# Kernel optimization log

Hardware: AMD Instinct MI355X
Metric: run time of the kernel (lower is better)

## Reference

```python
import math
import jax, jax.numpy as jnp
import numpy as np

NUM_HEADS = 12
EPS = 1e-4


def softmax_kernel_features(data, proj, is_query):
    # data: [B,H,N,d], proj: [m,d] -> features [B,H,N,m]
    d = data.shape[-1]
    data_normalizer = 1.0 / math.sqrt(math.sqrt(d))
    ratio = 1.0 / math.sqrt(proj.shape[0])
    data_dash = jnp.einsum('bhnd,md->bhnm', data_normalizer * data, proj)
    diag_data = (jnp.sum(jnp.square(data), axis=-1, keepdims=True)
                 * 0.5 * data_normalizer * data_normalizer)  # [B,H,N,1]
    if is_query:
        stab = jnp.max(data_dash, axis=-1, keepdims=True)
    else:
        stab = jnp.max(data_dash)
    return ratio * (jnp.exp(data_dash - diag_data - stab) + EPS)


def setup_inputs() -> dict:
    key = jax.random.key(0)
    k0, k1, k2, k3, k4 = jax.random.split(key, 5)
    B, N, C, H = 8, 4096, 768, NUM_HEADS
    hd = C // H
    m = int(hd * math.log(hd))  # 266
    x = jax.random.normal(k0, (B, N, C), dtype=jnp.float32)
    W_qkv = jax.random.normal(k1, (C, 3 * C), dtype=jnp.float32) / math.sqrt(C)
    W_proj = jax.random.normal(k2, (C, C), dtype=jnp.float32) / math.sqrt(C)
    b_proj = jnp.zeros((C,), dtype=jnp.float32)
    proj_mat = jax.random.normal(k3, (m, hd), dtype=jnp.float32)
    return {'x': x, 'W_qkv': W_qkv, 'W_proj': W_proj, 'b_proj': b_proj,
            'proj_mat': proj_mat}


def reference(x, W_qkv, W_proj, b_proj, proj_mat):
    B, N, C = x.shape
    H = NUM_HEADS
    hd = C // H
    qkv = (x @ W_qkv).reshape(B, N, 3, H, hd)
    qkv = jnp.transpose(qkv, (2, 0, 3, 1, 4))  # [3,B,H,N,hd]
    q, k, v = qkv[0], qkv[1], qkv[2]
    q1 = softmax_kernel_features(q, proj_mat, is_query=True)   # [B,H,N,m]
    k1 = softmax_kernel_features(k, proj_mat, is_query=False)  # [B,H,N,m]
    # FAVOR+ non-causal linear attention
    kv = jnp.einsum('bhnm,bhnd->bhmd', k1, v)        # [B,H,m,hd]
    ksum = jnp.sum(k1, axis=2)                        # [B,H,m]
    z = 1.0 / jnp.einsum('bhnm,bhm->bhn', q1, ksum)  # [B,H,N]
    out = jnp.einsum('bhnm,bhmd->bhnd', q1, kv) * z[..., None]
    out = jnp.transpose(out, (0, 2, 1, 3)).reshape(B, N, C)
    return out @ W_proj + b_proj
```

## Files before the change

kernel.cpp:

```cpp
#include <hip/hip_runtime.h>
#include <hip/hip_bf16.h>
#include <math.h>

#define B_ 8
#define N_TOK 4096
#define C_ 768
#define H_ 12
#define HD_ 64
#define M_ 266
#define TC_ 2304
#define BH_ 96
#define ROWS_ 32768

#define M2 288
#define MP 296
#define KVS 72
#define K1S 40

#define DN 0.35355339059327373f
#define RATIO 0.06131393394849658f
#define FEPS 1e-4f
#define NEG_INF -3.0e38f

typedef __attribute__((ext_vector_type(4))) float f32x4;
typedef __attribute__((ext_vector_type(8))) short bf16x8;

__device__ __forceinline__ float bf2f(unsigned short u) {
  return __uint_as_float(((unsigned int)u) << 16);
}
__device__ __forceinline__ unsigned short f2bf(float f) {
  unsigned int x = __float_as_uint(f);
  unsigned int r = (x + 0x7fffu + ((x >> 16) & 1u)) >> 16;
  return (unsigned short)r;
}

#define GLOAD_LDS16(g, l) \
  __builtin_amdgcn_global_load_lds( \
      (const __attribute__((address_space(1))) void*)(g), \
      (__attribute__((address_space(3))) void*)(l), 16, 0, 0)

__global__ __launch_bounds__(256) void cast_bf16(
    const float* __restrict__ src, unsigned short* __restrict__ dst, int n)
{
  int i = (blockIdx.x * 256 + threadIdx.x) * 4;
  if (i < n) {
    float4 v = *(const float4*)&src[i];
    ushort4 u;
    u.x = f2bf(v.x); u.y = f2bf(v.y); u.z = f2bf(v.z); u.w = f2bf(v.w);
    *(ushort4*)&dst[i] = u;
  }
}

__global__ __launch_bounds__(256) void cast_pbf(
    const float* __restrict__ P, unsigned short* __restrict__ Pbf)
{
  int idx = blockIdx.x * 256 + threadIdx.x;
  if (idx < M2 * 64) {
    int m = idx >> 6;
    Pbf[idx] = (m < M_) ? f2bf(P[idx]) : (unsigned short)0;
  }
}

__global__ __launch_bounds__(256) void transpose_cast(
    const float* __restrict__ src, unsigned short* __restrict__ dst,
    int R, int Ccols)
{
  __shared__ float t[32][33];
  const int c0 = blockIdx.x * 32, r0 = blockIdx.y * 32;
  const int tx = threadIdx.x & 31, ty = threadIdx.x >> 5;
#pragma unroll
  for (int i = 0; i < 32; i += 8)
    t[ty + i][tx] = src[(size_t)(r0 + ty + i) * Ccols + c0 + tx];
  __syncthreads();
#pragma unroll
  for (int i = 0; i < 32; i += 8)
    dst[(size_t)(c0 + ty + i) * R + r0 + tx] = f2bf(t[tx][ty + i]);
}

template <int NT, int C_BF16, int HAS_BIAS>
__global__ __launch_bounds__(512) void gemm_pipe(
    const unsigned short* __restrict__ A, const unsigned short* __restrict__ Bt,
    const float* __restrict__ bias, void* __restrict__ Cptr)
{
  __shared__ unsigned short lds_[73728];
  const int Kdim = 768, Ndim = NT * 128;
  const int tid = threadIdx.x;
  const int lane = tid & 63, w = tid >> 6;

  const int id = blockIdx.x;
  const int sid = (id & 7) * (16 * NT) + (id >> 3);
  const int row0 = (sid / NT) * 256;
  const int col0 = (sid % NT) * 128;

  const int srow = w * 8 + (lane >> 3);
  const int skb = (((lane & 7) ^ ((lane >> 3) & 7)) << 4);
  const size_t agb0 = (size_t)(row0 + srow) * Kdim + (skb >> 1);
  const size_t agb1 = (size_t)(row0 + 64 + srow) * Kdim + (skb >> 1);
  const size_t agb2 = (size_t)(row0 + 128 + srow) * Kdim + (skb >> 1);
  const size_t agb3 = (size_t)(row0 + 192 + srow) * Kdim + (skb >> 1);
  const size_t bgb0 = (size_t)(col0 + srow) * Kdim + (skb >> 1);
  const size_t bgb1 = (size_t)(col0 + 64 + srow) * Kdim + (skb >> 1);
  const int al0 = 0 * 4096 + w * 512 + lane * 8;
  const int al1 = 1 * 4096 + w * 512 + lane * 8;
  const int al2 = 2 * 4096 + w * 512 + lane * 8;
  const int al3 = 3 * 4096 + w * 512 + lane * 8;
  const int bl0 = 16384 + 0 * 4096 + w * 512 + lane * 8;
  const int bl1 = 16384 + 1 * 4096 + w * 512 + lane * 8;

#define STAGE_Q(tt) do { \
    unsigned short* Lq_ = lds_ + ((tt) % 3) * 24576; \
    const int kq_ = (tt) * 64; \
    GLOAD_LDS16(A + agb0 + kq_, Lq_ + al0); \
    GLOAD_LDS16(A + agb1 + kq_, Lq_ + al1); \
    GLOAD_LDS16(A + agb2 + kq_, Lq_ + al2); \
    GLOAD_LDS16(A + agb3 + kq_, Lq_ + al3); \
    GLOAD_LDS16(Bt + bgb0 + kq_, Lq_ + bl0); \
    GLOAD_LDS16(Bt + bgb1 + kq_, Lq_ + bl1); \
  } while (0)

  const int fr = lane & 15, q = lane >> 4;
  const int wm = w >> 2, wn = w & 3;
  const int f7 = fr & 7;
  const int sl0 = ((q + 0) ^ f7) << 3;
  const int sl1 = ((q + 4) ^ f7) << 3;
  const int abase = (wm * 128 + fr) * 64;
  const int bbase0 = 16384 + (wn * 32 + fr) * 64;
  const int bbase1 = 16384 + (wn * 32 + 16 + fr) * 64;

  f32x4 acc[8][2];
  const f32x4 fz = {0.f, 0.f, 0.f, 0.f};
#pragma unroll
  for (int m = 0; m < 8; ++m) { acc[m][0] = fz; acc[m][1] = fz; }

  STAGE_Q(0);
  STAGE_Q(1);

#pragma unroll 1
  for (int t = 0; t < 12; ++t) {
    if (t < 10) STAGE_Q(t + 2);
    if (t < 10)       asm volatile("s_waitcnt vmcnt(12)" ::: "memory");
    else if (t == 10) asm volatile("s_waitcnt vmcnt(6)" ::: "memory");
    else              asm volatile("s_waitcnt vmcnt(0)" ::: "memory");
    __builtin_amdgcn_sched_barrier(0);
    __builtin_amdgcn_s_barrier();
    __builtin_amdgcn_sched_barrier(0);

    const unsigned short* Lb = lds_ + (t % 3) * 24576;
#pragma unroll
    for (int ks = 0; ks < 2; ++ks) {
      const int sl = ks ? sl1 : sl0;
      bf16x8 bv0 = *(const bf16x8*)&Lb[bbase0 + sl];
      bf16x8 bv1 = *(const bf16x8*)&Lb[bbase1 + sl];
      bf16x8 av[8];
#pragma unroll
      for (int m = 0; m < 8; ++m)
        av[m] = *(const bf16x8*)&Lb[abase + m * 1024 + sl];
      __builtin_amdgcn_s_setprio(1);
#pragma unroll
      for (int m = 0; m < 8; ++m) {
        acc[m][0] = __builtin_amdgcn_mfma_f32_16x16x32_bf16(av[m], bv0, acc[m][0], 0, 0, 0);
        acc[m][1] = __builtin_amdgcn_mfma_f32_16x16x32_bf16(av[m], bv1, acc[m][1], 0, 0, 0);
      }
      __builtin_amdgcn_s_setprio(0);
    }
    __builtin_amdgcn_sched_barrier(0);
    __builtin_amdgcn_s_barrier();
    __builtin_amdgcn_sched_barrier(0);
  }
#undef STAGE_Q

  const int orow = q * 4;
#pragma unroll
  for (int m = 0; m < 8; ++m) {
#pragma unroll
    for (int n = 0; n < 2; ++n) {
      const int c = col0 + wn * 32 + n * 16 + fr;
      float badd = 0.f;
      if constexpr (HAS_BIAS) badd = bias[c];
#pragma unroll
      for (int j = 0; j < 4; ++j) {
        const int r = row0 + wm * 128 + m * 16 + orow + j;
        float v = acc[m][n][j] + badd;
        if constexpr (C_BF16)
          ((unsigned short*)Cptr)[(size_t)r * Ndim + c] = f2bf(v);
        else
          ((float*)Cptr)[(size_t)r * Ndim + c] = v;
      }
    }
  }
}

__global__ __launch_bounds__(256) void kmax_mfma(
    const unsigned short* __restrict__ qkv, const unsigned short* __restrict__ Pbf,
    float* __restrict__ bmax)
{
  __shared__ unsigned short K_lds[2][64 * KVS];
  __shared__ float red[4];
  const int tid = threadIdx.x;
  const int w = tid >> 6, lane = tid & 63;
  const int lr = lane & 15, q = lane >> 4;
  const int bh = blockIdx.x, chunk = blockIdx.y, z = blockIdx.z;
  const int b = bh / H_, h = bh % H_;
  const int ms = z * 8 + 2 * w;
  const int mc = (z == 1 && w == 3) ? 3 : 2;
  const int sn = 16 * w + (lane >> 2);
  const int sd0 = (lane & 3) * 16;
  const f32x4 fz = {0.f, 0.f, 0.f, 0.f};
  float mx = NEG_INF;

  bf16x8 pf0[3], pf1[3];
#pragma unroll
  for (int i = 0; i < 3; ++i) {
    const unsigned short* prow = Pbf + (size_t)((ms + i) * 16 + lr) * 64 + q * 8;
    pf0[i] = *(const bf16x8*)prow;
    pf1[i] = *(const bf16x8*)(prow + 32);
  }

  const unsigned short* kbase = qkv + (size_t)(b * N_TOK + chunk * 512 + sn) * TC_ + C_ + h * HD_ + sd0;
  const size_t gstep = (size_t)64 * TC_;

  int4 ka = *(const int4*)kbase;
  int4 kb = *(const int4*)(kbase + 8);
  *(int4*)&K_lds[0][sn * KVS + sd0] = ka;
  *(int4*)&K_lds[0][sn * KVS + sd0 + 8] = kb;
  asm volatile("s_waitcnt lgkmcnt(0)" ::: "memory");
  __builtin_amdgcn_s_barrier();

#pragma unroll 1
  for (int g = 0; g < 8; ++g) {
    const unsigned short* Kc = K_lds[g & 1];
    if (g < 7) {
      const unsigned short* kr = kbase + (size_t)(g + 1) * gstep;
      ka = *(const int4*)kr;
      kb = *(const int4*)(kr + 8);
    }
    __builtin_amdgcn_sched_barrier(0);
    bf16x8 bk[4][2];
#pragma unroll
    for (int nt = 0; nt < 4; ++nt) {
      bk[nt][0] = *(const bf16x8*)&Kc[(nt * 16 + lr) * KVS + q * 8];
      bk[nt][1] = *(const bf16x8*)&Kc[(nt * 16 + lr) * KVS + 32 + q * 8];
    }
#pragma unroll
    for (int i = 0; i < 3; ++i) {
      if (i >= mc) continue;
      const int m = (ms + i) * 16 + lr;
#pragma unroll
      for (int nt = 0; nt < 4; ++nt) {
        f32x4 s = fz;
        s = __builtin_amdgcn_mfma_f32_16x16x32_bf16(bk[nt][0], pf0[i], s, 0, 0, 0);
        s = __builtin_amdgcn_mfma_f32_16x16x32_bf16(bk[nt][1], pf1[i], s, 0, 0, 0);
        if (m < M_)
          mx = fmaxf(mx, fmaxf(fmaxf(s[0], s[1]), fmaxf(s[2], s[3])));
      }
    }
    if (g < 7) {
      __builtin_amdgcn_sched_barrier(0);
      __builtin_amdgcn_s_barrier();
      unsigned short* Kn = (unsigned short*)K_lds[(g & 1) ^ 1];
      *(int4*)&Kn[sn * KVS + sd0] = ka;
      *(int4*)&Kn[sn * KVS + sd0 + 8] = kb;
      asm volatile("s_waitcnt lgkmcnt(0)" ::: "memory");
      __builtin_amdgcn_sched_barrier(0);
      __builtin_amdgcn_s_barrier();
      __builtin_amdgcn_sched_barrier(0);
    }
  }
#pragma unroll
  for (int off = 32; off >= 1; off >>= 1) mx = fmaxf(mx, __shfl_xor(mx, off));
  if (lane == 0) red[w] = mx;
  __syncthreads();
  if (tid == 0)
    bmax[(z * 8 + chunk) * BH_ + bh] = fmaxf(fmaxf(red[0], red[1]), fmaxf(red[2], red[3]));
}

__global__ __launch_bounds__(256) void kmax_reduce(
    const float* __restrict__ bmax, float* __restrict__ kmaxp, int n)
{
  __shared__ float red[4];
  float v = NEG_INF;
  for (int i = threadIdx.x; i < n; i += 256) v = fmaxf(v, bmax[i]);
#pragma unroll
  for (int off = 32; off >= 1; off >>= 1) v = fmaxf(v, __shfl_xor(v, off));
  if ((threadIdx.x & 63) == 0) red[threadIdx.x >> 6] = v;
  __syncthreads();
  if (threadIdx.x == 0)
    kmaxp[0] = DN * fmaxf(fmaxf(red[0], red[1]), fmaxf(red[2], red[3]));
}

__global__ __launch_bounds__(256) void kv_partial_mfma(
    const unsigned short* __restrict__ qkv, const unsigned short* __restrict__ Pbf,
    const float* __restrict__ kmaxp,
    float* __restrict__ kvpart, float* __restrict__ ksumpart)
{
  __shared__ unsigned short K_lds[64 * KVS];
  __shared__ unsigned short Vt_lds[64 * KVS];
  __shared__ unsigned short k1_lds[272 * K1S];
  __shared__ float diag_lds[64];
  const int tid = threadIdx.x;
  const int w = tid >> 6, lane = tid & 63;
  const int lr = lane & 15, q = lane >> 4;
  const int bh = blockIdx.x, chunk = blockIdx.y, z = blockIdx.z;
  const int b = bh / H_, h = bh % H_;
  const float stab = kmaxp[0];
  const int ms = z * 8 + 2 * w;
  const int mc = (z == 1 && w == 3) ? 3 : 2;
  const int sn = 16 * w + (lane >> 2);
  const int sd0 = (lane & 3) * 16;
  const int vswz = sn ^ ((lane & 3) << 4);
  const int kswz = (lr >> 3) << 4;
  const f32x4 fz = {0.f, 0.f, 0.f, 0.f};

  f32x4 kvacc[3][4];
  float ksacc[3];
#pragma unroll
  for (int i = 0; i < 3; ++i) {
    ksacc[i] = 0.f;
#pragma unroll
    for (int dt = 0; dt < 4; ++dt) kvacc[i][dt] = fz;
  }

  bf16x8 pf0[3], pf1[3];
#pragma unroll
  for (int i = 0; i < 3; ++i) {
    const unsigned short* prow = Pbf + (size_t)((ms + i) * 16 + lr) * 64 + q * 8;
    pf0[i] = *(const bf16x8*)prow;
    pf1[i] = *(const bf16x8*)(prow + 32);
  }

  const unsigned short* kbase = qkv + (size_t)(b * N_TOK + chunk * 512 + sn) * TC_ + C_ + h * HD_ + sd0;
  const size_t gstep = (size_t)64 * TC_;

  auto write_buf = [&](int4 wka, int4 wkb, int4 wva, int4 wvb) {
    *(int4*)&K_lds[sn * KVS + sd0] = wka;
    *(int4*)&K_lds[sn * KVS + sd0 + 8] = wkb;
    float sq = 0.f;
    const unsigned short* pk0 = (const unsigned short*)&wka;
#pragma unroll
    for (int j = 0; j < 8; ++j) { float f = bf2f(pk0[j]); sq = fmaf(f, f, sq); }
    const unsigned short* pk1 = (const unsigned short*)&wkb;
#pragma unroll
    for (int j = 0; j < 8; ++j) { float f = bf2f(pk1[j]); sq = fmaf(f, f, sq); }
    sq += __shfl_xor(sq, 1);
    sq += __shfl_xor(sq, 2);
    if ((lane & 3) == 0) diag_lds[sn] = 0.0625f * sq;
    const unsigned short* pv0 = (const unsigned short*)&wva;
    const unsigned short* pv1 = (const unsigned short*)&wvb;
#pragma unroll
    for (int j = 0; j < 8; ++j) Vt_lds[(sd0 + j) * KVS + vswz] = pv0[j];
#pragma unroll
    for (int j = 0; j < 8; ++j) Vt_lds[(sd0 + 8 + j) * KVS + vswz] = pv1[j];
  };

  int4 ka = *(const int4*)kbase;
  int4 kb = *(const int4*)(kbase + 8);
  int4 va = *(const int4*)(kbase + C_);
  int4 vb = *(const int4*)(kbase + C_ + 8);
  write_buf(ka, kb, va, vb);
  asm volatile("s_waitcnt lgkmcnt(0)" ::: "memory");
  __builtin_amdgcn_s_barrier();

#pragma unroll 1
  for (int g = 0; g < 8; ++g) {
    if (g < 7) {
      const unsigned short* kr = kbase + (size_t)(g + 1) * gstep;
      ka = *(const int4*)kr;
      kb = *(const int4*)(kr + 8);
      va = *(const int4*)(kr + C_);
      vb = *(const int4*)(kr + C_ + 8);
    }
    __builtin_amdgcn_sched_barrier(0);

#pragma unroll
    for (int ks = 0; ks < 2; ++ks) {
      bf16x8 bkl[2][2];
#pragma unroll
      for (int t = 0; t < 2; ++t) {
        const int nrow = ((2 * ks + t) * 16 + lr) * KVS;
        bkl[t][0] = *(const bf16x8*)&K_lds[nrow + q * 8];
        bkl[t][1] = *(const bf16x8*)&K_lds[nrow + 32 + q * 8];
      }
      bf16x8 bv[4];
#pragma unroll
      for (int dt = 0; dt < 4; ++dt)
        bv[dt] = *(const bf16x8*)&Vt_lds[(dt * 16 + lr) * KVS + ((ks * 32 + q * 8) ^ (dt << 4))];

#pragma unroll
      for (int i = 0; i < 3; ++i) {
        if (i >= mc) continue;
        const int mt = ms + i;
        const int m = mt * 16 + lr;
        const int mrow = (mt * 16 + lr) * K1S;
        float loc = 0.f;
#pragma unroll
        for (int t = 0; t < 2; ++t) {
          f32x4 s = fz;
          s = __builtin_amdgcn_mfma_f32_16x16x32_bf16(bkl[t][0], pf0[i], s, 0, 0, 0);
          s = __builtin_amdgcn_mfma_f32_16x16x32_bf16(bkl[t][1], pf1[i], s, 0, 0, 0);
          ushort4 uo;
          unsigned short* puo = (unsigned short*)&uo;
#pragma unroll
          for (int j = 0; j < 4; ++j) {
            const int nl = (2 * ks + t) * 16 + q * 4 + j;
            float k1f = 0.f;
            if (m < M_) {
              float dash = DN * s[j];
              k1f = RATIO * (__expf(dash - diag_lds[nl] - stab) + FEPS);
            }
            loc += k1f;
            puo[j] = f2bf(k1f);
          }
          *(ushort4*)&k1_lds[mrow + ((t * 16 + q * 4) ^ kswz)] = uo;
        }
        ksacc[i] += loc;
        bf16x8 a1 = *(const bf16x8*)&k1_lds[mrow + ((q * 8) ^ kswz)];
#pragma unroll
        for (int dt = 0; dt < 4; ++dt)
          kvacc[i][dt] = __builtin_amdgcn_mfma_f32_16x16x32_bf16(a1, bv[dt], kvacc[i][dt], 0, 0, 0);
      }
    }

    if (g < 7) {
      __builtin_amdgcn_sched_barrier(0);
      __builtin_amdgcn_s_barrier();
      __builtin_amdgcn_sched_barrier(0);
      write_buf(ka, kb, va, vb);
      asm volatile("s_waitcnt lgkmcnt(0)" ::: "memory");
      __builtin_amdgcn_sched_barrier(0);
      __builtin_amdgcn_s_barrier();
      __builtin_amdgcn_sched_barrier(0);
    }
  }

  const size_t cb = (size_t)(chunk * BH_ + bh) * 64;
#pragma unroll
  for (int i = 0; i < 3; ++i) {
    if (i >= mc) continue;
    const int mt = ms + i;
#pragma unroll
    for (int dt = 0; dt < 4; ++dt) {
      float4 v4;
      v4.x = kvacc[i][dt][0]; v4.y = kvacc[i][dt][1];
      v4.z = kvacc[i][dt][2]; v4.w = kvacc[i][dt][3];
      *(float4*)&kvpart[(cb + dt * 16 + lr) * M2 + mt * 16 + q * 4] = v4;
    }
    float s = ksacc[i];
    s += __shfl_xor(s, 16);
    s += __shfl_xor(s, 32);
    if (lane < 16)
      ksumpart[(size_t)(chunk * BH_ + bh) * M2 + mt * 16 + lane] = s;
  }
}

__global__ __launch_bounds__(256) void kv_reduce2(
    const float* __restrict__ kvpart, const float* __restrict__ ksumpart,
    unsigned short* __restrict__ kvt_g, float* __restrict__ ksum_g)
{
  const int KVN = BH_ * 64 * M2;
  const int KSN = BH_ * M2;
  int idx = blockIdx.x * 256 + threadIdx.x;
  if (idx < KVN) {
    int m = idx % M2;
    float s = 0.f;
    if (m < M_) {
#pragma unroll
      for (int c = 0; c < 8; ++c) s += kvpart[(size_t)c * KVN + idx];
    }
    kvt_g[idx] = f2bf(s);
  } else if (idx < KVN + KSN) {
    int j = idx - KVN;
    int m = j % M2;
    float s = 0.f;
    if (m < M_) {
#pragma unroll
      for (int c = 0; c < 8; ++c) s += ksumpart[(size_t)c * KSN + j];
    }
    ksum_g[j] = s;
  }
}

__global__ __launch_bounds__(256) void attn_mfma(
    const unsigned short* __restrict__ qkv, const unsigned short* __restrict__ Pbf,
    const unsigned short* __restrict__ kvt_g, const float* __restrict__ ksum_g,
    unsigned short* __restrict__ attn)
{
  __shared__ unsigned short q1_lds[64 * MP];
  __shared__ unsigned short kvt_lds[64 * MP];
  __shared__ float ksum_lds[M2];
  __shared__ float z_lds[64];
  const int tid = threadIdx.x;
  const int bh = blockIdx.x, qt = blockIdx.y;
  const int b = bh / H_, h = bh % H_;
  const int n0 = qt * 64;
  const int w = tid >> 6, lane = tid & 63;
  const int lr = lane & 15, q = lane >> 4;

  {
    const unsigned short* src = kvt_g + (size_t)bh * 64 * M2;
#pragma unroll
    for (int i = 0; i < 9; ++i) {
      int chunk = i * 256 + tid;
      int r = chunk / 36, c = (chunk % 36) * 8;
      *(int4*)&kvt_lds[r * MP + c] = *(const int4*)(src + r * M2 + c);
    }
    if (tid < 72)
      *(float4*)&ksum_lds[tid * 4] = *(const float4*)(ksum_g + (size_t)bh * M2 + tid * 4);
    if (tid < 64) {
      const int4 z4 = {0, 0, 0, 0};
      *(int4*)&q1_lds[tid * MP + 272] = z4;
      *(int4*)&q1_lds[tid * MP + 280] = z4;
    }
  }
  __syncthreads();

  const unsigned short* qrow = qkv + (size_t)(b * N_TOK + n0 + w * 16 + lr) * TC_ + h * HD_;
  bf16x8 bq0 = *(const bf16x8*)(qrow + q * 8);
  bf16x8 bq1 = *(const bf16x8*)(qrow + q * 8 + 32);
  float sq = 0.f;
  {
    const unsigned short* p0 = (const unsigned short*)&bq0;
    const unsigned short* p1 = (const unsigned short*)&bq1;
#pragma unroll
    for (int j = 0; j < 8; ++j) { float f = bf2f(p0[j]); sq = fmaf(f, f, sq); }
#pragma unroll
    for (int j = 0; j < 8; ++j) { float f = bf2f(p1[j]); sq = fmaf(f, f, sq); }
  }
  sq += __shfl_xor(sq, 16);
  sq += __shfl_xor(sq, 32);
  const float diag = 0.0625f * sq;

  f32x4 sacc[17];
  const f32x4 fz = {0.f, 0.f, 0.f, 0.f};
#pragma unroll
  for (int mt = 0; mt < 17; ++mt) sacc[mt] = fz;
#pragma unroll
  for (int mt = 0; mt < 17; ++mt) {
    const unsigned short* prow = Pbf + (size_t)(mt * 16 + lr) * 64;
    bf16x8 ap0 = *(const bf16x8*)(prow + q * 8);
    bf16x8 ap1 = *(const bf16x8*)(prow + q * 8 + 32);
    sacc[mt] = __builtin_amdgcn_mfma_f32_16x16x32_bf16(ap0, bq0, sacc[mt], 0, 0, 0);
    sacc[mt] = __builtin_amdgcn_mfma_f32_16x16x32_bf16(ap1, bq1, sacc[mt], 0, 0, 0);
  }

  float mxr = NEG_INF;
#pragma unroll
  for (int mt = 0; mt < 17; ++mt) {
#pragma unroll
    for (int j = 0; j < 4; ++j) {
      int m = mt * 16 + q * 4 + j;
      if (m < M_) mxr = fmaxf(mxr, sacc[mt][j]);
    }
  }
  mxr = fmaxf(mxr, __shfl_xor(mxr, 16));
  mxr = fmaxf(mxr, __shfl_xor(mxr, 32));
  const float mxd = DN * mxr;

  float zp = 0.f;
#pragma unroll
  for (int mt = 0; mt < 17; ++mt) {
    ushort4 uo;
    unsigned short* puo = (unsigned short*)&uo;
#pragma unroll
    for (int j = 0; j < 4; ++j) {
      const int m = mt * 16 + q * 4 + j;
      float q1f = 0.f;
      if (m < M_) {
        float dash = DN * sacc[mt][j];
        q1f = RATIO * (__expf(dash - diag - mxd) + FEPS);
      }
      zp = fmaf(q1f, ksum_lds[m], zp);
      puo[j] = f2bf(q1f);
    }
    *(ushort4*)&q1_lds[(w * 16 + lr) * MP + mt * 16 + q * 4] = uo;
  }
  zp += __shfl_xor(zp, 16);
  zp += __shfl_xor(zp, 32);
  if (q == 0) z_lds[w * 16 + lr] = 1.0f / zp;

  f32x4 oacc[4];
#pragma unroll
  for (int dt = 0; dt < 4; ++dt) oacc[dt] = fz;
#pragma unroll
  for (int ks = 0; ks < 9; ++ks) {
    bf16x8 aq = *(const bf16x8*)&q1_lds[(w * 16 + lr) * MP + ks * 32 + q * 8];
#pragma unroll
    for (int dt = 0; dt < 4; ++dt) {
      bf16x8 bkv = *(const bf16x8*)&kvt_lds[(dt * 16 + lr) * MP + ks * 32 + q * 8];
      oacc[dt] = __builtin_amdgcn_mfma_f32_16x16x32_bf16(aq, bkv, oacc[dt], 0, 0, 0);
    }
  }

  float zz[4];
#pragma unroll
  for (int j = 0; j < 4; ++j) zz[j] = z_lds[w * 16 + q * 4 + j];
#pragma unroll
  for (int dt = 0; dt < 4; ++dt) {
#pragma unroll
    for (int j = 0; j < 4; ++j) {
      const int r = b * N_TOK + n0 + w * 16 + q * 4 + j;
      attn[(size_t)r * C_ + h * HD_ + dt * 16 + lr] = f2bf(oacc[dt][j] * zz[j]);
    }
  }
}

extern "C" void kernel_launch(void* const* d_in, const int* in_sizes, int n_in,
                              void* d_out, int out_size, void* d_ws, size_t ws_size,
                              hipStream_t stream) {
  const float* x     = (const float*)d_in[0];
  const float* Wqkv  = (const float*)d_in[1];
  const float* Wproj = (const float*)d_in[2];
  const float* bproj = (const float*)d_in[3];
  const float* P     = (const float*)d_in[4];
  float* out = (float*)d_out;
  float* ws = (float*)d_ws;

  unsigned short* qkv    = (unsigned short*)ws;
  unsigned short* xb     = (unsigned short*)(ws + 37748736);
  float*          kvpart = ws + 37748736;
  unsigned short* attn   = (unsigned short*)(ws + 37748736);
  float* ksumpart = ws + 51904512;
  unsigned short* kvt_g  = (unsigned short*)(ws + 52125696);
  float* ksum_g   = ws + 53010432;
  float* bmax     = ws + 53038080;
  float* kmaxp    = ws + 53041152;
  unsigned short* Pbf    = (unsigned short*)(ws + 53041216);
  unsigned short* Wqkvt  = (unsigned short*)(ws + 53050432);
  unsigned short* Wprojt = (unsigned short*)(ws + 53935168);

  cast_bf16<<<dim3(24576), 256, 0, stream>>>(x, xb, ROWS_ * C_);
  transpose_cast<<<dim3(72, 24), 256, 0, stream>>>(Wqkv, Wqkvt, C_, TC_);
  transpose_cast<<<dim3(24, 24), 256, 0, stream>>>(Wproj, Wprojt, C_, C_);
  cast_pbf<<<dim3(72), 256, 0, stream>>>(P, Pbf);

  gemm_pipe<18, 1, 0><<<dim3(2304), 512, 0, stream>>>(xb, Wqkvt, nullptr, qkv);
  kmax_mfma<<<dim3(96, 8, 2), 256, 0, stream>>>(qkv, Pbf, bmax);
  kmax_reduce<<<dim3(1), 256, 0, stream>>>(bmax, kmaxp, 1536);
  kv_partial_mfma<<<dim3(96, 8, 2), 256, 0, stream>>>(qkv, Pbf, kmaxp, kvpart, ksumpart);
  kv_reduce2<<<dim3(7020), 256, 0, stream>>>(kvpart, ksumpart, kvt_g, ksum_g);
  attn_mfma<<<dim3(96, 64), 256, 0, stream>>>(qkv, Pbf, kvt_g, ksum_g, attn);
  gemm_pipe<6, 0, 1><<<dim3(768), 512, 0, stream>>>(attn, Wprojt, bproj, out);
}
```

Before: 539.3 us.

## Widen GEMM tiles to 256x256 with double-buffered LDS staging

```diff
diff --git a/kernel.cpp b/kernel.cpp
--- a/kernel.cpp
+++ b/kernel.cpp
@@ -82,40 +82,40 @@
     const unsigned short* __restrict__ A, const unsigned short* __restrict__ Bt,
     const float* __restrict__ bias, void* __restrict__ Cptr)
 {
-  __shared__ unsigned short lds_[73728];
-  const int Kdim = 768, Ndim = NT * 128;
+  __shared__ unsigned short lds_[65536];
+  const int Kdim = 768, Ndim = NT * 256;
   const int tid = threadIdx.x;
   const int lane = tid & 63, w = tid >> 6;
 
   const int id = blockIdx.x;
-  const int sid = (id & 7) * (16 * NT) + (id >> 3);
+  const int nwg8 = (128 * NT) >> 3;
+  const int sid = (id & 7) * nwg8 + (id >> 3);
   const int row0 = (sid / NT) * 256;
-  const int col0 = (sid % NT) * 128;
-
-  const int srow = w * 8 + (lane >> 3);
-  const int skb = (((lane & 7) ^ ((lane >> 3) & 7)) << 4);
-  const size_t agb0 = (size_t)(row0 + srow) * Kdim + (skb >> 1);
-  const size_t agb1 = (size_t)(row0 + 64 + srow) * Kdim + (skb >> 1);
-  const size_t agb2 = (size_t)(row0 + 128 + srow) * Kdim + (skb >> 1);
-  const size_t agb3 = (size_t)(row0 + 192 + srow) * Kdim + (skb >> 1);
-  const size_t bgb0 = (size_t)(col0 + srow) * Kdim + (skb >> 1);
-  const size_t bgb1 = (size_t)(col0 + 64 + srow) * Kdim + (skb >> 1);
-  const int al0 = 0 * 4096 + w * 512 + lane * 8;
-  const int al1 = 1 * 4096 + w * 512 + lane * 8;
-  const int al2 = 2 * 4096 + w * 512 + lane * 8;
-  const int al3 = 3 * 4096 + w * 512 + lane * 8;
-  const int bl0 = 16384 + 0 * 4096 + w * 512 + lane * 8;
-  const int bl1 = 16384 + 1 * 4096 + w * 512 + lane * 8;
+  const int col0 = (sid % NT) * 256;
+
+  const int srow = tid >> 3;
+  const int skb = (((tid & 7) ^ (srow & 7)) << 4);
+  const size_t ag0 = (size_t)(row0 + srow) * Kdim + (skb >> 1);
+  const size_t ag1 = (size_t)(row0 + 64 + srow) * Kdim + (skb >> 1);
+  const size_t ag2 = (size_t)(row0 + 128 + srow) * Kdim + (skb >> 1);
+  const size_t ag3 = (size_t)(row0 + 192 + srow) * Kdim + (skb >> 1);
+  const size_t bg0 = (size_t)(col0 + srow) * Kdim + (skb >> 1);
+  const size_t bg1 = (size_t)(col0 + 64 + srow) * Kdim + (skb >> 1);
+  const size_t bg2 = (size_t)(col0 + 128 + srow) * Kdim + (skb >> 1);
+  const size_t bg3 = (size_t)(col0 + 192 + srow) * Kdim + (skb >> 1);
+  const int dst = tid * 8;
 
 #define STAGE_Q(tt) do { \
-    unsigned short* Lq_ = lds_ + ((tt) % 3) * 24576; \
+    unsigned short* Lq_ = lds_ + ((tt) & 1) * 32768; \
     const int kq_ = (tt) * 64; \
-    GLOAD_LDS16(A + agb0 + kq_, Lq_ + al0); \
-    GLOAD_LDS16(A + agb1 + kq_, Lq_ + al1); \
-    GLOAD_LDS16(A + agb2 + kq_, Lq_ + al2); \
-    GLOAD_LDS16(A + agb3 + kq_, Lq_ + al3); \
-    GLOAD_LDS16(Bt + bgb0 + kq_, Lq_ + bl0); \
-    GLOAD_LDS16(Bt + bgb1 + kq_, Lq_ + bl1); \
+    GLOAD_LDS16(A + ag0 + kq_, Lq_ + 0 * 4096 + dst); \
+    GLOAD_LDS16(A + ag1 + kq_, Lq_ + 1 * 4096 + dst); \
+    GLOAD_LDS16(A + ag2 + kq_, Lq_ + 2 * 4096 + dst); \
+    GLOAD_LDS16(A + ag3 + kq_, Lq_ + 3 * 4096 + dst); \
+    GLOAD_LDS16(Bt + bg0 + kq_, Lq_ + 16384 + 0 * 4096 + dst); \
+    GLOAD_LDS16(Bt + bg1 + kq_, Lq_ + 16384 + 1 * 4096 + dst); \
+    GLOAD_LDS16(Bt + bg2 + kq_, Lq_ + 16384 + 2 * 4096 + dst); \
+    GLOAD_LDS16(Bt + bg3 + kq_, Lq_ + 16384 + 3 * 4096 + dst); \
   } while (0)
 
   const int fr = lane & 15, q = lane >> 4;
@@ -124,43 +124,46 @@
   const int sl0 = ((q + 0) ^ f7) << 3;
   const int sl1 = ((q + 4) ^ f7) << 3;
   const int abase = (wm * 128 + fr) * 64;
-  const int bbase0 = 16384 + (wn * 32 + fr) * 64;
-  const int bbase1 = 16384 + (wn * 32 + 16 + fr) * 64;
-
-  f32x4 acc[8][2];
+  const int bbase = 16384 + (wn * 64 + fr) * 64;
+
+  f32x4 acc[8][4];
   const f32x4 fz = {0.f, 0.f, 0.f, 0.f};
 #pragma unroll
-  for (int m = 0; m < 8; ++m) { acc[m][0] = fz; acc[m][1] = fz; }
+  for (int m = 0; m < 8; ++m)
+#pragma unroll
+    for (int n = 0; n < 4; ++n) acc[m][n] = fz;
 
   STAGE_Q(0);
-  STAGE_Q(1);
 
 #pragma unroll 1
   for (int t = 0; t < 12; ++t) {
-    if (t < 10) STAGE_Q(t + 2);
-    if (t < 10)       asm volatile("s_waitcnt vmcnt(12)" ::: "memory");
-    else if (t == 10) asm volatile("s_waitcnt vmcnt(6)" ::: "memory");
-    else              asm volatile("s_waitcnt vmcnt(0)" ::: "memory");
+    if (t < 11) {
+      STAGE_Q(t + 1);
+      asm volatile("s_waitcnt vmcnt(8)" ::: "memory");
+    } else {
+      asm volatile("s_waitcnt vmcnt(0)" ::: "memory");
+    }
     __builtin_amdgcn_sched_barrier(0);
     __builtin_amdgcn_s_barrier();
     __builtin_amdgcn_sched_barrier(0);
 
-    const unsigned short* Lb = lds_ + (t % 3) * 24576;
+    const unsigned short* Lb = lds_ + (t & 1) * 32768;
 #pragma unroll
     for (int ks = 0; ks < 2; ++ks) {
       const int sl = ks ? sl1 : sl0;
-      bf16x8 bv0 = *(const bf16x8*)&Lb[bbase0 + sl];
-      bf16x8 bv1 = *(const bf16x8*)&Lb[bbase1 + sl];
-      bf16x8 av[8];
+      bf16x8 av[8], bv[4];
 #pragma unroll
       for (int m = 0; m < 8; ++m)
         av[m] = *(const bf16x8*)&Lb[abase + m * 1024 + sl];
+#pragma unroll
+      for (int n = 0; n < 4; ++n)
+        bv[n] = *(const bf16x8*)&Lb[bbase + n * 1024 + sl];
       __builtin_amdgcn_s_setprio(1);
 #pragma unroll
-      for (int m = 0; m < 8; ++m) {
-        acc[m][0] = __builtin_amdgcn_mfma_f32_16x16x32_bf16(av[m], bv0, acc[m][0], 0, 0, 0);
-        acc[m][1] = __builtin_amdgcn_mfma_f32_16x16x32_bf16(av[m], bv1, acc[m][1], 0, 0, 0);
-      }
+      for (int m = 0; m < 8; ++m)
+#pragma unroll
+        for (int n = 0; n < 4; ++n)
+          acc[m][n] = __builtin_amdgcn_mfma_f32_16x16x32_bf16(av[m], bv[n], acc[m][n], 0, 0, 0);
       __builtin_amdgcn_s_setprio(0);
     }
     __builtin_amdgcn_sched_barrier(0);
@@ -173,8 +176,8 @@
 #pragma unroll
   for (int m = 0; m < 8; ++m) {
 #pragma unroll
-    for (int n = 0; n < 2; ++n) {
-      const int c = col0 + wn * 32 + n * 16 + fr;
+    for (int n = 0; n < 4; ++n) {
+      const int c = col0 + wn * 64 + n * 16 + fr;
       float badd = 0.f;
       if constexpr (HAS_BIAS) badd = bias[c];
 #pragma unroll
@@ -632,11 +635,11 @@
   transpose_cast<<<dim3(24, 24), 256, 0, stream>>>(Wproj, Wprojt, C_, C_);
   cast_pbf<<<dim3(72), 256, 0, stream>>>(P, Pbf);
 
-  gemm_pipe<18, 1, 0><<<dim3(2304), 512, 0, stream>>>(xb, Wqkvt, nullptr, qkv);
+  gemm_pipe<9, 1, 0><<<dim3(1152), 512, 0, stream>>>(xb, Wqkvt, nullptr, qkv);
   kmax_mfma<<<dim3(96, 8, 2), 256, 0, stream>>>(qkv, Pbf, bmax);
   kmax_reduce<<<dim3(1), 256, 0, stream>>>(bmax, kmaxp, 1536);
   kv_partial_mfma<<<dim3(96, 8, 2), 256, 0, stream>>>(qkv, Pbf, kmaxp, kvpart, ksumpart);
   kv_reduce2<<<dim3(7020), 256, 0, stream>>>(kvpart, ksumpart, kvt_g, ksum_g);
   attn_mfma<<<dim3(96, 64), 256, 0, stream>>>(qkv, Pbf, kvt_g, ksum_g, attn);
-  gemm_pipe<6, 0, 1><<<dim3(768), 512, 0, stream>>>(attn, Wprojt, bproj, out);
-}
+  gemm_pipe<3, 0, 1><<<dim3(384), 512, 0, stream>>>(attn, Wprojt, bproj, out);
+}
```

After: 521.0 us. -3.4%, faster.
